# Performance work log

Hardware: AMD Instinct MI355X
Metric: run time of the kernel (lower is better)

## Reference

```python
import jax, jax.numpy as jnp
import numpy as np

NEG_INF = -1.0e9  # matches torch masked_fill value


def setup_inputs() -> dict:
    key = jax.random.key(0)
    k1, k2, k3, k4 = jax.random.split(key, 4)
    B, S, H = 32, 4096, 1024
    query = jax.random.normal(k1, (B, 1, H), dtype=jnp.float32)
    keys = jax.random.normal(k2, (B, S, H), dtype=jnp.float32)
    src_mask = jax.random.randint(k3, (B, S), 0, 2) == 1
    # nn.Linear weight [out,in]; y = x @ W.T
    W_query = jax.random.normal(k4, (H, H), dtype=jnp.float32) * (1.0 / np.sqrt(H))
    return {"query": query, "keys": keys, "src_mask": src_mask, "W_query": W_query}


def reference(query, keys, src_mask, W_query):
    # projected query: [B,1,H] @ W.T -> [B,1,H]
    q = jnp.einsum("bqh,oh->bqo", query, W_query)
    # scores: [B,S] (single query squeezed)
    scores = jnp.einsum("bqh,bsh->bqs", q, keys)[:, 0, :]
    scores = jnp.where(src_mask, NEG_INF, scores)
    weights = jax.nn.softmax(scores, axis=-1)[:, None, :]  # [B,1,S]
    context = jnp.einsum("bqs,bsh->bqh", weights, keys)    # [B,1,H]
    return (context, weights)
```

## Files before the change

### kernel.cpp

```cpp
#include <hip/hip_runtime.h>
#include <math.h>

#define BB 32
#define SS 4096
#define HH 1024
#define NCHUNK 16
#define CHUNK (SS / NCHUNK)
#define NEG_INF9 (-1.0e9f)

__device__ __forceinline__ float wave_reduce_sum(float v) {
#pragma unroll
    for (int off = 32; off > 0; off >>= 1) v += __shfl_xor(v, off, 64);
    return v;
}

__global__ __launch_bounds__(256) void qproj_kernel(const float* __restrict__ query,
                                                    const float* __restrict__ W,
                                                    float* __restrict__ q) {
    const int b    = blockIdx.y;
    const int wave = threadIdx.x >> 6;
    const int lane = threadIdx.x & 63;

    const float4* qp = (const float4*)(query + (size_t)b * HH);
    float4 qv[4];
#pragma unroll
    for (int r = 0; r < 4; ++r) qv[r] = qp[r * 64 + lane];

    const int obase = blockIdx.x * 128 + wave * 32;
    for (int i = 0; i < 32; ++i) {
        const int o = obase + i;
        const float4* wp = (const float4*)(W + (size_t)o * HH);
        float acc = 0.f;
#pragma unroll
        for (int r = 0; r < 4; ++r) {
            const float4 wv = wp[r * 64 + lane];
            acc += wv.x * qv[r].x + wv.y * qv[r].y + wv.z * qv[r].z + wv.w * qv[r].w;
        }
        acc = wave_reduce_sum(acc);
        if (lane == 0) q[(size_t)b * HH + o] = acc;
    }
}

__global__ __launch_bounds__(256) void attn_chunk_kernel(const float* __restrict__ q,
                                                         const float* __restrict__ keys,
                                                         const int* __restrict__ mask,
                                                         float* __restrict__ raw_scores,
                                                         float* __restrict__ pm,
                                                         float* __restrict__ pl,
                                                         float* __restrict__ pO) {
    const int b    = blockIdx.y;
    const int c    = blockIdx.x;
    const int wave = threadIdx.x >> 6;
    const int lane = threadIdx.x & 63;

    const float4* qp = (const float4*)(q + (size_t)b * HH);
    float4 qv[4];
#pragma unroll
    for (int r = 0; r < 4; ++r) qv[r] = qp[r * 64 + lane];

    float m = -INFINITY;
    float l = 0.f;
    float4 acc[4];
#pragma unroll
    for (int r = 0; r < 4; ++r) acc[r] = make_float4(0.f, 0.f, 0.f, 0.f);

    const int s0 = c * CHUNK;
    for (int t = wave; t < CHUNK; t += 4) {
        const int s = s0 + t;
        const float4* kp = (const float4*)(keys + ((size_t)b * SS + s) * HH);
        float4 kv[4];
#pragma unroll
        for (int r = 0; r < 4; ++r) kv[r] = kp[r * 64 + lane];

        float sc = 0.f;
#pragma unroll
        for (int r = 0; r < 4; ++r)
            sc += kv[r].x * qv[r].x + kv[r].y * qv[r].y + kv[r].z * qv[r].z + kv[r].w * qv[r].w;
        sc = wave_reduce_sum(sc);

        if (mask[(size_t)b * SS + s] != 0) sc = NEG_INF9;
        if (lane == 0) raw_scores[(size_t)b * SS + s] = sc;

        const float mnew  = fmaxf(m, sc);
        const float scale = __expf(m - mnew);
        const float p     = __expf(sc - mnew);
        l = l * scale + p;
#pragma unroll
        for (int r = 0; r < 4; ++r) {
            acc[r].x = acc[r].x * scale + p * kv[r].x;
            acc[r].y = acc[r].y * scale + p * kv[r].y;
            acc[r].z = acc[r].z * scale + p * kv[r].z;
            acc[r].w = acc[r].w * scale + p * kv[r].w;
        }
        m = mnew;
    }

    __shared__ float  sm[4];
    __shared__ float  sl[4];
    __shared__ float4 sO[4][256];
#pragma unroll
    for (int r = 0; r < 4; ++r) sO[wave][r * 64 + lane] = acc[r];
    if (lane == 0) { sm[wave] = m; sl[wave] = l; }
    __syncthreads();

    const float M = fmaxf(fmaxf(sm[0], sm[1]), fmaxf(sm[2], sm[3]));
    float f[4];
#pragma unroll
    for (int w = 0; w < 4; ++w) f[w] = __expf(sm[w] - M);
    const float L = sl[0] * f[0] + sl[1] * f[1] + sl[2] * f[2] + sl[3] * f[3];

    const int tid = threadIdx.x;
    float4 o = make_float4(0.f, 0.f, 0.f, 0.f);
#pragma unroll
    for (int w = 0; w < 4; ++w) {
        const float4 v = sO[w][tid];
        o.x += f[w] * v.x; o.y += f[w] * v.y; o.z += f[w] * v.z; o.w += f[w] * v.w;
    }
    ((float4*)(pO + ((size_t)b * NCHUNK + c) * HH))[tid] = o;
    if (tid == 0) { pm[b * NCHUNK + c] = M; pl[b * NCHUNK + c] = L; }
}

__global__ __launch_bounds__(256) void combine_kernel(const float* __restrict__ pm,
                                                      const float* __restrict__ pl,
                                                      const float* __restrict__ pO,
                                                      float* __restrict__ context,
                                                      float* __restrict__ weights) {
    const int b   = blockIdx.x;
    const int tid = threadIdx.x;

    float M = -INFINITY;
#pragma unroll
    for (int c = 0; c < NCHUNK; ++c) M = fmaxf(M, pm[b * NCHUNK + c]);
    float fc[NCHUNK];
    float L = 0.f;
#pragma unroll
    for (int c = 0; c < NCHUNK; ++c) {
        fc[c] = __expf(pm[b * NCHUNK + c] - M);
        L += pl[b * NCHUNK + c] * fc[c];
    }
    const float invL = 1.f / L;

    float4 o = make_float4(0.f, 0.f, 0.f, 0.f);
#pragma unroll
    for (int c = 0; c < NCHUNK; ++c) {
        const float4 v = ((const float4*)(pO + ((size_t)b * NCHUNK + c) * HH))[tid];
        const float g = fc[c] * invL;
        o.x += g * v.x; o.y += g * v.y; o.z += g * v.z; o.w += g * v.w;
    }
    ((float4*)(context + (size_t)b * HH))[tid] = o;

    for (int s = tid; s < SS; s += 256) {
        const float sc = weights[(size_t)b * SS + s];
        weights[(size_t)b * SS + s] = __expf(sc - M) * invL;
    }
}

extern "C" void kernel_launch(void* const* d_in, const int* in_sizes, int n_in,
                              void* d_out, int out_size, void* d_ws, size_t ws_size,
                              hipStream_t stream) {
    const float* query = (const float*)d_in[0];
    const float* keys  = (const float*)d_in[1];
    const int*   mask  = (const int*)d_in[2];
    const float* W     = (const float*)d_in[3];

    float* context = (float*)d_out;
    float* weights = (float*)d_out + (size_t)BB * HH;

    float* q  = (float*)d_ws;
    float* pm = q + (size_t)BB * HH;
    float* pl = pm + BB * NCHUNK;
    float* pO = pl + BB * NCHUNK;

    qproj_kernel<<<dim3(HH / 128, BB), 256, 0, stream>>>(query, W, q);
    attn_chunk_kernel<<<dim3(NCHUNK, BB), 256, 0, stream>>>(q, keys, mask, weights, pm, pl, pO);
    combine_kernel<<<BB, 256, 0, stream>>>(pm, pl, pO, context, weights);
}
```

Baseline: 711.1 us.

## Double-buffer key loads, process two rows per wave, and double chunk count

The attention chunk kernel now has each wave handle two key rows per iteration. It prefetches the next pair of rows into registers while computing the current pair, and fuses the two score reductions into one shuffle loop. NCHUNK doubles to 32 and qproj uses smaller per-block output tiles, giving more blocks in flight on the bandwidth-bound key stream. In exchange, register pressure roughly doubles, which launch_bounds(256,4) may force into spills, and the combine step has more partials to merge.

```diff
diff --git a/kernel.cpp b/kernel.cpp
--- a/kernel.cpp
+++ b/kernel.cpp
@@ -4,7 +4,7 @@
 #define BB 32
 #define SS 4096
 #define HH 1024
-#define NCHUNK 16
+#define NCHUNK 32
 #define CHUNK (SS / NCHUNK)
 #define NEG_INF9 (-1.0e9f)
 
@@ -12,6 +12,16 @@
 #pragma unroll
     for (int off = 32; off > 0; off >>= 1) v += __shfl_xor(v, off, 64);
     return v;
+}
+
+__device__ __forceinline__ void wave_reduce_sum2(float& a, float& b) {
+#pragma unroll
+    for (int off = 32; off > 0; off >>= 1) {
+        const float ta = __shfl_xor(a, off, 64);
+        const float tb = __shfl_xor(b, off, 64);
+        a += ta;
+        b += tb;
+    }
 }
 
 __global__ __launch_bounds__(256) void qproj_kernel(const float* __restrict__ query,
@@ -26,8 +36,8 @@
 #pragma unroll
     for (int r = 0; r < 4; ++r) qv[r] = qp[r * 64 + lane];
 
-    const int obase = blockIdx.x * 128 + wave * 32;
-    for (int i = 0; i < 32; ++i) {
+    const int obase = blockIdx.x * 64 + wave * 16;
+    for (int i = 0; i < 16; ++i) {
         const int o = obase + i;
         const float4* wp = (const float4*)(W + (size_t)o * HH);
         float acc = 0.f;
@@ -41,13 +51,13 @@
     }
 }
 
-__global__ __launch_bounds__(256) void attn_chunk_kernel(const float* __restrict__ q,
-                                                         const float* __restrict__ keys,
-                                                         const int* __restrict__ mask,
-                                                         float* __restrict__ raw_scores,
-                                                         float* __restrict__ pm,
-                                                         float* __restrict__ pl,
-                                                         float* __restrict__ pO) {
+__global__ __launch_bounds__(256, 4) void attn_chunk_kernel(const float* __restrict__ q,
+                                                            const float* __restrict__ keys,
+                                                            const int* __restrict__ mask,
+                                                            float* __restrict__ raw_scores,
+                                                            float* __restrict__ pm,
+                                                            float* __restrict__ pl,
+                                                            float* __restrict__ pO) {
     const int b    = blockIdx.y;
     const int c    = blockIdx.x;
     const int wave = threadIdx.x >> 6;
@@ -64,35 +74,59 @@
 #pragma unroll
     for (int r = 0; r < 4; ++r) acc[r] = make_float4(0.f, 0.f, 0.f, 0.f);
 
-    const int s0 = c * CHUNK;
-    for (int t = wave; t < CHUNK; t += 4) {
-        const int s = s0 + t;
-        const float4* kp = (const float4*)(keys + ((size_t)b * SS + s) * HH);
-        float4 kv[4];
-#pragma unroll
-        for (int r = 0; r < 4; ++r) kv[r] = kp[r * 64 + lane];
-
-        float sc = 0.f;
-#pragma unroll
-        for (int r = 0; r < 4; ++r)
-            sc += kv[r].x * qv[r].x + kv[r].y * qv[r].y + kv[r].z * qv[r].z + kv[r].w * qv[r].w;
-        sc = wave_reduce_sum(sc);
-
-        if (mask[(size_t)b * SS + s] != 0) sc = NEG_INF9;
-        if (lane == 0) raw_scores[(size_t)b * SS + s] = sc;
-
-        const float mnew  = fmaxf(m, sc);
+    const size_t bbase = (size_t)b * SS;
+    const int s0 = c * CHUNK + wave * 2;
+
+    float4 kva[4], kvb[4];
+    {
+        const float4* kp0 = (const float4*)(keys + (bbase + s0) * HH);
+        const float4* kp1 = (const float4*)(keys + (bbase + s0 + 1) * HH);
+#pragma unroll
+        for (int r = 0; r < 4; ++r) { kva[r] = kp0[r * 64 + lane]; kvb[r] = kp1[r * 64 + lane]; }
+    }
+
+    const int NIT = CHUNK / 8;
+    for (int i = 0; i < NIT; ++i) {
+        const int s = s0 + 8 * i;
+
+        const int sn = (i + 1 < NIT) ? (s + 8) : s;
+        float4 kna[4], knb[4];
+        {
+            const float4* kp0 = (const float4*)(keys + (bbase + sn) * HH);
+            const float4* kp1 = (const float4*)(keys + (bbase + sn + 1) * HH);
+#pragma unroll
+            for (int r = 0; r < 4; ++r) { kna[r] = kp0[r * 64 + lane]; knb[r] = kp1[r * 64 + lane]; }
+        }
+
+        float sc0 = 0.f, sc1 = 0.f;
+#pragma unroll
+        for (int r = 0; r < 4; ++r) {
+            sc0 += kva[r].x * qv[r].x + kva[r].y * qv[r].y + kva[r].z * qv[r].z + kva[r].w * qv[r].w;
+            sc1 += kvb[r].x * qv[r].x + kvb[r].y * qv[r].y + kvb[r].z * qv[r].z + kvb[r].w * qv[r].w;
+        }
+        wave_reduce_sum2(sc0, sc1);
+
+        const int2 mk = *(const int2*)(mask + bbase + s);
+        if (mk.x != 0) sc0 = NEG_INF9;
+        if (mk.y != 0) sc1 = NEG_INF9;
+        if (lane == 0) *(float2*)(raw_scores + bbase + s) = make_float2(sc0, sc1);
+
+        const float mnew  = fmaxf(m, fmaxf(sc0, sc1));
         const float scale = __expf(m - mnew);
-        const float p     = __expf(sc - mnew);
-        l = l * scale + p;
+        const float p0    = __expf(sc0 - mnew);
+        const float p1    = __expf(sc1 - mnew);
+        l = l * scale + p0 + p1;
 #pragma unroll
         for (int r = 0; r < 4; ++r) {
-            acc[r].x = acc[r].x * scale + p * kv[r].x;
-            acc[r].y = acc[r].y * scale + p * kv[r].y;
-            acc[r].z = acc[r].z * scale + p * kv[r].z;
-            acc[r].w = acc[r].w * scale + p * kv[r].w;
+            acc[r].x = acc[r].x * scale + p0 * kva[r].x + p1 * kvb[r].x;
+            acc[r].y = acc[r].y * scale + p0 * kva[r].y + p1 * kvb[r].y;
+            acc[r].z = acc[r].z * scale + p0 * kva[r].z + p1 * kvb[r].z;
+            acc[r].w = acc[r].w * scale + p0 * kva[r].w + p1 * kvb[r].w;
         }
         m = mnew;
+
+#pragma unroll
+        for (int r = 0; r < 4; ++r) { kva[r] = kna[r]; kvb[r] = knb[r]; }
     }
 
     __shared__ float  sm[4];
@@ -171,7 +205,7 @@
     float* pl = pm + BB * NCHUNK;
     float* pO = pl + BB * NCHUNK;
 
-    qproj_kernel<<<dim3(HH / 128, BB), 256, 0, stream>>>(query, W, q);
+    qproj_kernel<<<dim3(HH / 64, BB), 256, 0, stream>>>(query, W, q);
     attn_chunk_kernel<<<dim3(NCHUNK, BB), 256, 0, stream>>>(q, keys, mask, weights, pm, pl, pO);
     combine_kernel<<<BB, 256, 0, stream>>>(pm, pl, pO, context, weights);
 }
```

Measured after the change: 725.0 us. Within noise of the previous version (+2.0%).
